# Performance work log

Measured on AMD Instinct MI355X. Metric: run time of the kernel, lower is better.

Reference implementation:

```python
import jax, jax.numpy as jnp
import numpy as np

N = 100000
E = 1600000
IN_C = 128
HID = 128
NUM_CLASSES = 16


def setup_inputs() -> dict:
    key = jax.random.key(0)
    ks = jax.random.split(key, 8)
    x = jax.random.normal(ks[0], (N, IN_C), dtype=jnp.float32)
    edge_index = jax.random.randint(ks[1], (2, E), 0, N, dtype=jnp.int64)
    s1 = 1.0 / np.sqrt(IN_C)
    s2 = 1.0 / np.sqrt(HID)
    W1 = jax.random.uniform(ks[2], (IN_C, HID), jnp.float32, -s1, s1)
    b1 = jnp.zeros((HID,), jnp.float32)
    W2 = jax.random.uniform(ks[3], (HID, HID), jnp.float32, -s2, s2)
    b2 = jnp.zeros((HID,), jnp.float32)
    Wl = jax.random.uniform(ks[4], (HID, NUM_CLASSES), jnp.float32, -s2, s2)
    bl = jax.random.uniform(ks[5], (NUM_CLASSES,), jnp.float32, -s2, s2)
    return {"x": x, "edge_index": edge_index, "W1": W1, "b1": b1,
            "W2": W2, "b2": b2, "Wl": Wl, "bl": bl}


def gcn_conv(x, src, dst, norm, W, b, n_nodes):
    # x: [N, F_in]; src/dst: [E+N] (self-loops appended); norm: [E+N]
    h = x @ W  # [N, F_out] -- transform first (F_out <= F_in style), then gather
    msg = h[src] * norm[:, None]  # [E+N, F_out] gathered, normalized messages
    out = jax.ops.segment_sum(msg, dst, num_segments=n_nodes)  # scatter-add
    return out + b


def reference(x, edge_index, W1, b1, W2, b2, Wl, bl):
    loop = jnp.arange(N, dtype=edge_index.dtype)
    src = jnp.concatenate([edge_index[0], loop])  # add self-loops
    dst = jnp.concatenate([edge_index[1], loop])
    # symmetric GCN normalization: deg computed on target side incl. self-loops
    deg = jax.ops.segment_sum(jnp.ones_like(dst, dtype=x.dtype), dst,
                              num_segments=N)
    dinv = jnp.where(deg > 0, jax.lax.rsqrt(deg), 0.0)
    norm = dinv[src] * dinv[dst]  # [E+N]

    h = jax.nn.relu(gcn_conv(x, src, dst, norm, W1, b1, N))
    h = jax.nn.relu(gcn_conv(h, src, dst, norm, W2, b2, N))
    logits = h @ Wl + bl
    return jax.nn.softmax(logits, axis=1)
```

## Files before the change

kernel.cpp:

```cpp
#include <hip/hip_runtime.h>
#include <hip/hip_fp16.h>

#define FDIM 128
#define NCLS 16

#define SCAN_T 256
#define SCAN_I 8
#define SCAN_CHUNK (SCAN_T * SCAN_I)

typedef _Float16 f16x8 __attribute__((ext_vector_type(8)));
typedef float f32x4 __attribute__((ext_vector_type(4)));

__global__ void k_count(const int* __restrict__ dst, int* cnt, int e) {
    int i = blockIdx.x * blockDim.x + threadIdx.x;
    if (i < e) atomicAdd(&cnt[dst[i]], 1);
}

__global__ __launch_bounds__(SCAN_T) void k_scan1(const int* __restrict__ cnt,
                                                  int* __restrict__ excl,
                                                  int* __restrict__ blockSum,
                                                  float* __restrict__ dinv, int n) {
    __shared__ int ts[SCAN_T];
    int b = blockIdx.x, t = threadIdx.x;
    int base = b * SCAN_CHUNK + t * SCAN_I;
    int v[SCAN_I];
    int s = 0;
    #pragma unroll
    for (int i = 0; i < SCAN_I; ++i) {
        int idx = base + i;
        v[i] = (idx < n) ? cnt[idx] : 0;
        if (idx < n) dinv[idx] = rsqrtf((float)(v[i] + 1));
        s += v[i];
    }
    ts[t] = s;
    __syncthreads();
    for (int off = 1; off < SCAN_T; off <<= 1) {
        int x = (t >= off) ? ts[t - off] : 0;
        __syncthreads();
        ts[t] += x;
        __syncthreads();
    }
    int ex = (t == 0) ? 0 : ts[t - 1];
    #pragma unroll
    for (int i = 0; i < SCAN_I; ++i) {
        int idx = base + i;
        if (idx < n) excl[idx] = ex;
        ex += v[i];
    }
    if (t == SCAN_T - 1) blockSum[b] = ts[SCAN_T - 1];
}

__global__ __launch_bounds__(1024) void k_scan2(int* blockSum, int* total, int nb) {
    __shared__ int ts[1024];
    int t = threadIdx.x;
    int v = (t < nb) ? blockSum[t] : 0;
    ts[t] = v;
    __syncthreads();
    for (int off = 1; off < 1024; off <<= 1) {
        int x = (t >= off) ? ts[t - off] : 0;
        __syncthreads();
        ts[t] += x;
        __syncthreads();
    }
    if (t < nb) blockSum[t] = (t == 0) ? 0 : ts[t - 1];
    if (t == 1023) *total = ts[1023];
}

__global__ void k_scan3(int* __restrict__ row_ptr, int* __restrict__ cursor,
                        const int* __restrict__ blockSum, const int* __restrict__ total,
                        int n) {
    int i = blockIdx.x * blockDim.x + threadIdx.x;
    if (i < n) {
        int v = row_ptr[i] + blockSum[i / SCAN_CHUNK];
        row_ptr[i] = v;
        cursor[i] = v;
    }
    if (i == 0) row_ptr[n] = *total;
}

__global__ void k_scatter(const int* __restrict__ src, const int* __restrict__ dst,
                          int* cursor, int* __restrict__ csr_off, int e) {
    int i = blockIdx.x * blockDim.x + threadIdx.x;
    if (i >= e) return;
    int pos = atomicAdd(&cursor[dst[i]], 1);
    csr_off[pos] = src[i] << 8;
}

__global__ __launch_bounds__(256) void k_prepw(const float* __restrict__ W1,
                                               const float* __restrict__ W2,
                                               __half* __restrict__ T1,
                                               __half* __restrict__ T2) {
    const float* W = (blockIdx.x == 0) ? W1 : W2;
    __half* T = (blockIdx.x == 0) ? T1 : T2;
    int t = threadIdx.x;
    for (int i = t; i < 128 * 32; i += 256) {
        int c = i >> 5, k4 = (i & 31) * 4;
        float a = W[(k4 + 0) * 128 + c];
        float b = W[(k4 + 1) * 128 + c];
        float d = W[(k4 + 2) * 128 + c];
        float f = W[(k4 + 3) * 128 + c];
        __half2 h0 = __float22half2_rn(make_float2(a, b));
        __half2 h1 = __float22half2_rn(make_float2(d, f));
        uint2 u;
        u.x = *reinterpret_cast<unsigned int*>(&h0);
        u.y = *reinterpret_cast<unsigned int*>(&h1);
        *reinterpret_cast<uint2*>(&T[c * 128 + k4]) = u;
    }
}

template <typename T>
__global__ __launch_bounds__(512) void k_gemm_mfma(const T* __restrict__ A,
                                                   const __half* __restrict__ WT,
                                                   const float* __restrict__ dinv,
                                                   __half* __restrict__ C, int n) {
    __shared__ _Float16 as[128 * 128];
    __shared__ _Float16 wt[128 * 128];
    int t = threadIdx.x;
    int r0 = blockIdx.x * 128;

    for (int i = t; i < 2048; i += 512) {
        int c = i >> 4, k8 = i & 15;
        uint4 u = reinterpret_cast<const uint4*>(WT)[i];
        int byte = (c * 256 + k8 * 16) ^ ((c & 7) << 4);
        *reinterpret_cast<uint4*>(reinterpret_cast<char*>(wt) + byte) = u;
    }

    if constexpr (sizeof(T) == 4) {
        for (int i = t; i < 128 * 16; i += 512) {
            int r = i >> 4, c8 = i & 15;
            float4 v0 = make_float4(0.f, 0.f, 0.f, 0.f);
            float4 v1 = make_float4(0.f, 0.f, 0.f, 0.f);
            if (r0 + r < n) {
                v0 = reinterpret_cast<const float4*>(A)[(size_t)(r0 + r) * 32 + c8 * 2];
                v1 = reinterpret_cast<const float4*>(A)[(size_t)(r0 + r) * 32 + c8 * 2 + 1];
            }
            __half2 h0 = __float22half2_rn(make_float2(v0.x, v0.y));
            __half2 h1 = __float22half2_rn(make_float2(v0.z, v0.w));
            __half2 h2 = __float22half2_rn(make_float2(v1.x, v1.y));
            __half2 h3 = __float22half2_rn(make_float2(v1.z, v1.w));
            uint4 u;
            u.x = *reinterpret_cast<unsigned int*>(&h0);
            u.y = *reinterpret_cast<unsigned int*>(&h1);
            u.z = *reinterpret_cast<unsigned int*>(&h2);
            u.w = *reinterpret_cast<unsigned int*>(&h3);
            int byte = (r * 256 + c8 * 16) ^ ((r & 7) << 4);
            *reinterpret_cast<uint4*>(reinterpret_cast<char*>(as) + byte) = u;
        }
    } else {
        for (int i = t; i < 128 * 16; i += 512) {
            int r = i >> 4, c8 = i & 15;
            uint4 u = make_uint4(0, 0, 0, 0);
            if (r0 + r < n)
                u = reinterpret_cast<const uint4*>(A)[(size_t)(r0 + r) * 16 + c8];
            int byte = (r * 256 + c8 * 16) ^ ((r & 7) << 4);
            *reinterpret_cast<uint4*>(reinterpret_cast<char*>(as) + byte) = u;
        }
    }
    __syncthreads();

    int w = t >> 6, l = t & 63;
    int lrow = l & 15, lk = l >> 4;
    int rw = w * 16;

    f16x8 afrag[4];
    #pragma unroll
    for (int ks = 0; ks < 4; ++ks) {
        int row = rw + lrow;
        int byte = (row * 256 + (ks * 4 + lk) * 16) ^ ((row & 7) << 4);
        afrag[ks] = *reinterpret_cast<const f16x8*>(reinterpret_cast<const char*>(as) + byte);
    }
    float dv[4];
    #pragma unroll
    for (int reg = 0; reg < 4; ++reg) {
        int rg = r0 + rw + lk * 4 + reg;
        dv[reg] = (rg < n) ? dinv[rg] : 0.f;
    }

    #pragma unroll
    for (int ct = 0; ct < 8; ++ct) {
        f32x4 acc = {0.f, 0.f, 0.f, 0.f};
        #pragma unroll
        for (int ks = 0; ks < 4; ++ks) {
            int c = ct * 16 + lrow;
            int byte = (c * 256 + (ks * 4 + lk) * 16) ^ ((c & 7) << 4);
            f16x8 bfrag = *reinterpret_cast<const f16x8*>(reinterpret_cast<const char*>(wt) + byte);
            acc = __builtin_amdgcn_mfma_f32_16x16x32_f16(afrag[ks], bfrag, acc, 0, 0, 0);
        }
        #pragma unroll
        for (int reg = 0; reg < 4; ++reg) {
            int rg = r0 + rw + lk * 4 + reg;
            if (rg < n)
                C[(size_t)rg * FDIM + ct * 16 + lrow] = __float2half(acc[reg] * dv[reg]);
        }
    }
}

template <bool FUSE>
__global__ __launch_bounds__(256) void k_agg2e(const __half* __restrict__ Y,
                                               const int* __restrict__ csr_off,
                                               const int* __restrict__ row_ptr,
                                               const float* __restrict__ dinv,
                                               const float* __restrict__ bias,
                                               const float* __restrict__ Wl,
                                               const float* __restrict__ bl,
                                               __half* __restrict__ hout,
                                               float* __restrict__ out, int n) {
    __shared__ float s_wl[NCLS * FDIM];
    __shared__ float s_bl[NCLS];
    if (FUSE) {
        for (int i = threadIdx.x; i < FDIM * NCLS / 4; i += 256) {
            int k = i >> 2, c4 = (i & 3) * 4;
            float4 v = reinterpret_cast<const float4*>(Wl)[i];
            s_wl[(c4 + 0) * FDIM + k] = v.x;
            s_wl[(c4 + 1) * FDIM + k] = v.y;
            s_wl[(c4 + 2) * FDIM + k] = v.z;
            s_wl[(c4 + 3) * FDIM + k] = v.w;
        }
        if (threadIdx.x < NCLS) s_bl[threadIdx.x] = bl[threadIdx.x];
        __syncthreads();
    }

    int node = blockIdx.x * 4 + (threadIdx.x >> 6);
    if (node >= n) return;
    int lane = threadIdx.x & 63;
    int half = lane >> 5, l32 = lane & 31;
    const char* Yb = reinterpret_cast<const char*>(Y);
    const char* lanebase = Yb + (l32 << 3);

    float a0 = 0.f, a1 = 0.f, a2 = 0.f, a3 = 0.f;
    int beg = row_ptr[node], end = row_ptr[node + 1];

    for (int j0 = beg; j0 < end; j0 += 64) {
        int cnt = min(64, end - j0);
        int myoff = (j0 + lane < end) ? csr_off[j0 + lane] : 0;
        int k = 0;
        for (; k + 8 <= cnt; k += 8) {
            uint2 u[4];
            #pragma unroll
            for (int i = 0; i < 4; ++i) {
                int oe = __builtin_amdgcn_readlane(myoff, k + 2 * i);
                int oo = __builtin_amdgcn_readlane(myoff, k + 2 * i + 1);
                int off = half ? oo : oe;
                u[i] = *reinterpret_cast<const uint2*>(lanebase + off);
            }
            __half2* p = reinterpret_cast<__half2*>(u);
            __half2 lo = __hadd2(__hadd2(p[0], p[2]), __hadd2(p[4], p[6]));
            __half2 hi = __hadd2(__hadd2(p[1], p[3]), __hadd2(p[5], p[7]));
            float2 flo = __half22float2(lo), fhi = __half22float2(hi);
            a0 += flo.x; a1 += flo.y; a2 += fhi.x; a3 += fhi.y;
        }
        for (; k + 2 <= cnt; k += 2) {
            int oe = __builtin_amdgcn_readlane(myoff, k);
            int oo = __builtin_amdgcn_readlane(myoff, k + 1);
            int off = half ? oo : oe;
            uint2 u = *reinterpret_cast<const uint2*>(lanebase + off);
            __half2* p = reinterpret_cast<__half2*>(&u);
            float2 flo = __half22float2(p[0]), fhi = __half22float2(p[1]);
            a0 += flo.x; a1 += flo.y; a2 += fhi.x; a3 += fhi.y;
        }
        if (k < cnt) {
            int o = __builtin_amdgcn_readlane(myoff, k);
            uint2 u = *reinterpret_cast<const uint2*>(lanebase + o);
            __half2* p = reinterpret_cast<__half2*>(&u);
            float sel = (half == 0) ? 1.0f : 0.0f;
            float2 flo = __half22float2(p[0]), fhi = __half22float2(p[1]);
            a0 += flo.x * sel; a1 += flo.y * sel;
            a2 += fhi.x * sel; a3 += fhi.y * sel;
        }
    }

    a0 += __shfl_xor(a0, 32, 64);
    a1 += __shfl_xor(a1, 32, 64);
    a2 += __shfl_xor(a2, 32, 64);
    a3 += __shfl_xor(a3, 32, 64);

    uint2 su = *reinterpret_cast<const uint2*>(Yb + ((size_t)node << 8) + (l32 << 3));
    __half2* sp = reinterpret_cast<__half2*>(&su);
    float2 slo = __half22float2(sp[0]), shi = __half22float2(sp[1]);
    a0 += slo.x; a1 += slo.y; a2 += shi.x; a3 += shi.y;

    float di = dinv[node];
    float4 b = *reinterpret_cast<const float4*>(bias + l32 * 4);
    float h0 = fmaxf(a0 * di + b.x, 0.f);
    float h1 = fmaxf(a1 * di + b.y, 0.f);
    float h2 = fmaxf(a2 * di + b.z, 0.f);
    float h3 = fmaxf(a3 * di + b.w, 0.f);

    if (!FUSE) {
        if (half == 0) {
            __half2 o0 = __float22half2_rn(make_float2(h0, h1));
            __half2 o1 = __float22half2_rn(make_float2(h2, h3));
            uint2 o;
            o.x = *reinterpret_cast<unsigned int*>(&o0);
            o.y = *reinterpret_cast<unsigned int*>(&o1);
            *reinterpret_cast<uint2*>(reinterpret_cast<char*>(hout) + ((size_t)node << 8) + (l32 << 3)) = o;
        }
    } else {
        float lg[NCLS];
        #pragma unroll
        for (int c = 0; c < NCLS; ++c) {
            float4 w4 = *reinterpret_cast<const float4*>(&s_wl[c * FDIM + l32 * 4]);
            lg[c] = h0 * w4.x + h1 * w4.y + h2 * w4.z + h3 * w4.w;
        }
        #pragma unroll
        for (int off = 1; off < 32; off <<= 1) {
            #pragma unroll
            for (int c = 0; c < NCLS; ++c) lg[c] += __shfl_xor(lg[c], off, 64);
        }
        #pragma unroll
        for (int c = 0; c < NCLS; ++c) lg[c] += s_bl[c];
        float m = lg[0];
        #pragma unroll
        for (int c = 1; c < NCLS; ++c) m = fmaxf(m, lg[c]);
        float ev[NCLS];
        float sum = 0.f;
        #pragma unroll
        for (int c = 0; c < NCLS; ++c) { ev[c] = __expf(lg[c] - m); sum += ev[c]; }
        float inv = 1.0f / sum;
        float mye = 0.f;
        #pragma unroll
        for (int c = 0; c < NCLS; ++c) if (lane == c) mye = ev[c];
        if (lane < NCLS) out[(size_t)node * NCLS + lane] = mye * inv;
    }
}

extern "C" void kernel_launch(void* const* d_in, const int* in_sizes, int n_in,
                              void* d_out, int out_size, void* d_ws, size_t ws_size,
                              hipStream_t stream) {
    const float* x  = (const float*)d_in[0];
    const int*   ei = (const int*)d_in[1];
    const float* W1 = (const float*)d_in[2];
    const float* b1 = (const float*)d_in[3];
    const float* W2 = (const float*)d_in[4];
    const float* b2 = (const float*)d_in[5];
    const float* Wl = (const float*)d_in[6];
    const float* bl = (const float*)d_in[7];
    float* out = (float*)d_out;

    int n = in_sizes[0] / FDIM;
    int e = in_sizes[1] / 2;
    const int* src = ei;
    const int* dst = ei + e;

    int nb = (n + SCAN_CHUNK - 1) / SCAN_CHUNK;

    float* dinv    = (float*)d_ws;
    int*   cnt     = (int*)(dinv + n);
    int*   row_ptr = cnt + n;
    int*   cursor  = row_ptr + n + 1;
    int*   blockSum= cursor + n;
    int*   total   = blockSum + 1024;
    int*   csr_off = total + 1;
    uintptr_t p = (uintptr_t)(csr_off + e);
    p = (p + 15) & ~(uintptr_t)15;
    __half* wt1 = (__half*)p;
    __half* wt2 = wt1 + 128 * 128;
    __half* bufA = wt2 + 128 * 128;
    __half* bufB = bufA + (size_t)n * FDIM;

    int bn = (n + 255) / 256;
    int be = (e + 255) / 256;

    hipMemsetAsync(cnt, 0, (size_t)n * sizeof(int), stream);
    k_prepw<<<2, 256, 0, stream>>>(W1, W2, wt1, wt2);
    k_count<<<be, 256, 0, stream>>>(dst, cnt, e);
    k_scan1<<<nb, SCAN_T, 0, stream>>>(cnt, row_ptr, blockSum, dinv, n);
    k_scan2<<<1, 1024, 0, stream>>>(blockSum, total, nb);
    k_scan3<<<bn, 256, 0, stream>>>(row_ptr, cursor, blockSum, total, n);
    k_scatter<<<be, 256, 0, stream>>>(src, dst, cursor, csr_off, e);

    int bg = (n + 127) / 128;
    int ba = (n + 3) / 4;

    k_gemm_mfma<float><<<bg, 512, 0, stream>>>(x, wt1, dinv, bufA, n);
    k_agg2e<false><<<ba, 256, 0, stream>>>(bufA, csr_off, row_ptr, dinv, b1, Wl, bl, bufB, out, n);

    k_gemm_mfma<__half><<<bg, 512, 0, stream>>>(bufB, wt2, dinv, bufA, n);
    k_agg2e<true><<<ba, 256, 0, stream>>>(bufA, csr_off, row_ptr, dinv, b2, Wl, bl, bufB, out, n);
}
```

Before: 478.0 us.

## Gather four edges per wavefront with 16-byte loads and fold weight prep into scan

The aggregation kernel now splits each 64-lane wavefront into four 16-lane groups, each loading a full 256-byte fp16 row with 16-byte loads. Four neighbors are processed at once instead of two, with a two-step xor-shuffle reduction across groups at the end. The goal is fewer, wider gather instructions and more memory-level parallelism per wave on the edge-gather path. Separately, the weight transpose/fp16 conversion kernel is merged into the single-block scan2 launch as extra blocks, removing one kernel launch. The tail handling duplicates loads for masked groups, and the logits reduction now uses 16-lane shuffles.

```diff
diff --git a/kernel.cpp b/kernel.cpp
--- a/kernel.cpp
+++ b/kernel.cpp
@@ -50,20 +50,42 @@
     if (t == SCAN_T - 1) blockSum[b] = ts[SCAN_T - 1];
 }
 
-__global__ __launch_bounds__(1024) void k_scan2(int* blockSum, int* total, int nb) {
-    __shared__ int ts[1024];
-    int t = threadIdx.x;
-    int v = (t < nb) ? blockSum[t] : 0;
-    ts[t] = v;
-    __syncthreads();
-    for (int off = 1; off < 1024; off <<= 1) {
-        int x = (t >= off) ? ts[t - off] : 0;
+__global__ __launch_bounds__(1024) void k_scan2_prepw(int* blockSum, int* total, int nb,
+                                                      const float* __restrict__ W1,
+                                                      const float* __restrict__ W2,
+                                                      __half* __restrict__ T1,
+                                                      __half* __restrict__ T2) {
+    if (blockIdx.x == 0) {
+        __shared__ int ts[1024];
+        int t = threadIdx.x;
+        int v = (t < nb) ? blockSum[t] : 0;
+        ts[t] = v;
         __syncthreads();
-        ts[t] += x;
-        __syncthreads();
-    }
-    if (t < nb) blockSum[t] = (t == 0) ? 0 : ts[t - 1];
-    if (t == 1023) *total = ts[1023];
+        for (int off = 1; off < 1024; off <<= 1) {
+            int x = (t >= off) ? ts[t - off] : 0;
+            __syncthreads();
+            ts[t] += x;
+            __syncthreads();
+        }
+        if (t < nb) blockSum[t] = (t == 0) ? 0 : ts[t - 1];
+        if (t == 1023) *total = ts[1023];
+    } else {
+        const float* W = (blockIdx.x == 1) ? W1 : W2;
+        __half* T = (blockIdx.x == 1) ? T1 : T2;
+        for (int i = threadIdx.x; i < 128 * 32; i += 1024) {
+            int c = i >> 5, k4 = (i & 31) * 4;
+            float a = W[(k4 + 0) * 128 + c];
+            float b = W[(k4 + 1) * 128 + c];
+            float d = W[(k4 + 2) * 128 + c];
+            float f = W[(k4 + 3) * 128 + c];
+            __half2 h0 = __float22half2_rn(make_float2(a, b));
+            __half2 h1 = __float22half2_rn(make_float2(d, f));
+            uint2 u;
+            u.x = *reinterpret_cast<unsigned int*>(&h0);
+            u.y = *reinterpret_cast<unsigned int*>(&h1);
+            *reinterpret_cast<uint2*>(&T[c * 128 + k4]) = u;
+        }
+    }
 }
 
 __global__ void k_scan3(int* __restrict__ row_ptr, int* __restrict__ cursor,
@@ -84,28 +106,6 @@
     if (i >= e) return;
     int pos = atomicAdd(&cursor[dst[i]], 1);
     csr_off[pos] = src[i] << 8;
-}
-
-__global__ __launch_bounds__(256) void k_prepw(const float* __restrict__ W1,
-                                               const float* __restrict__ W2,
-                                               __half* __restrict__ T1,
-                                               __half* __restrict__ T2) {
-    const float* W = (blockIdx.x == 0) ? W1 : W2;
-    __half* T = (blockIdx.x == 0) ? T1 : T2;
-    int t = threadIdx.x;
-    for (int i = t; i < 128 * 32; i += 256) {
-        int c = i >> 5, k4 = (i & 31) * 4;
-        float a = W[(k4 + 0) * 128 + c];
-        float b = W[(k4 + 1) * 128 + c];
-        float d = W[(k4 + 2) * 128 + c];
-        float f = W[(k4 + 3) * 128 + c];
-        __half2 h0 = __float22half2_rn(make_float2(a, b));
-        __half2 h1 = __float22half2_rn(make_float2(d, f));
-        uint2 u;
-        u.x = *reinterpret_cast<unsigned int*>(&h0);
-        u.y = *reinterpret_cast<unsigned int*>(&h1);
-        *reinterpret_cast<uint2*>(&T[c * 128 + k4]) = u;
-    }
 }
 
 template <typename T>
@@ -196,7 +196,7 @@
 }
 
 template <bool FUSE>
-__global__ __launch_bounds__(256) void k_agg2e(const __half* __restrict__ Y,
+__global__ __launch_bounds__(256) void k_agg4e(const __half* __restrict__ Y,
                                                const int* __restrict__ csr_off,
                                                const int* __restrict__ row_ptr,
                                                const float* __restrict__ dinv,
@@ -223,11 +223,11 @@
     int node = blockIdx.x * 4 + (threadIdx.x >> 6);
     if (node >= n) return;
     int lane = threadIdx.x & 63;
-    int half = lane >> 5, l32 = lane & 31;
+    int grp = lane >> 4, l16 = lane & 15;
     const char* Yb = reinterpret_cast<const char*>(Y);
-    const char* lanebase = Yb + (l32 << 3);
-
-    float a0 = 0.f, a1 = 0.f, a2 = 0.f, a3 = 0.f;
+    const char* lanebase = Yb + l16 * 16;
+
+    float2 A0 = {0.f, 0.f}, A1 = {0.f, 0.f}, A2 = {0.f, 0.f}, A3 = {0.f, 0.f};
     int beg = row_ptr[node], end = row_ptr[node + 1];
 
     for (int j0 = beg; j0 < end; j0 += 64) {
@@ -235,75 +235,98 @@
         int myoff = (j0 + lane < end) ? csr_off[j0 + lane] : 0;
         int k = 0;
         for (; k + 8 <= cnt; k += 8) {
-            uint2 u[4];
-            #pragma unroll
-            for (int i = 0; i < 4; ++i) {
-                int oe = __builtin_amdgcn_readlane(myoff, k + 2 * i);
-                int oo = __builtin_amdgcn_readlane(myoff, k + 2 * i + 1);
-                int off = half ? oo : oe;
-                u[i] = *reinterpret_cast<const uint2*>(lanebase + off);
-            }
-            __half2* p = reinterpret_cast<__half2*>(u);
-            __half2 lo = __hadd2(__hadd2(p[0], p[2]), __hadd2(p[4], p[6]));
-            __half2 hi = __hadd2(__hadd2(p[1], p[3]), __hadd2(p[5], p[7]));
-            float2 flo = __half22float2(lo), fhi = __half22float2(hi);
-            a0 += flo.x; a1 += flo.y; a2 += fhi.x; a3 += fhi.y;
-        }
-        for (; k + 2 <= cnt; k += 2) {
-            int oe = __builtin_amdgcn_readlane(myoff, k);
-            int oo = __builtin_amdgcn_readlane(myoff, k + 1);
-            int off = half ? oo : oe;
-            uint2 u = *reinterpret_cast<const uint2*>(lanebase + off);
+            int o1 = __shfl(myoff, k + grp, 64);
+            int o2 = __shfl(myoff, k + 4 + grp, 64);
+            uint4 u1 = *reinterpret_cast<const uint4*>(lanebase + o1);
+            uint4 u2 = *reinterpret_cast<const uint4*>(lanebase + o2);
+            __half2* p1 = reinterpret_cast<__half2*>(&u1);
+            __half2* p2 = reinterpret_cast<__half2*>(&u2);
+            __half2 s0 = __hadd2(p1[0], p2[0]);
+            __half2 s1 = __hadd2(p1[1], p2[1]);
+            __half2 s2 = __hadd2(p1[2], p2[2]);
+            __half2 s3 = __hadd2(p1[3], p2[3]);
+            float2 f0 = __half22float2(s0), f1 = __half22float2(s1);
+            float2 f2 = __half22float2(s2), f3 = __half22float2(s3);
+            A0.x += f0.x; A0.y += f0.y; A1.x += f1.x; A1.y += f1.y;
+            A2.x += f2.x; A2.y += f2.y; A3.x += f3.x; A3.y += f3.y;
+        }
+        for (; k + 4 <= cnt; k += 4) {
+            int o = __shfl(myoff, k + grp, 64);
+            uint4 u = *reinterpret_cast<const uint4*>(lanebase + o);
             __half2* p = reinterpret_cast<__half2*>(&u);
-            float2 flo = __half22float2(p[0]), fhi = __half22float2(p[1]);
-            a0 += flo.x; a1 += flo.y; a2 += fhi.x; a3 += fhi.y;
+            float2 f0 = __half22float2(p[0]), f1 = __half22float2(p[1]);
+            float2 f2 = __half22float2(p[2]), f3 = __half22float2(p[3]);
+            A0.x += f0.x; A0.y += f0.y; A1.x += f1.x; A1.y += f1.y;
+            A2.x += f2.x; A2.y += f2.y; A3.x += f3.x; A3.y += f3.y;
         }
         if (k < cnt) {
-            int o = __builtin_amdgcn_readlane(myoff, k);
-            uint2 u = *reinterpret_cast<const uint2*>(lanebase + o);
+            int rem = cnt - k;
+            int o = __shfl(myoff, k + min(grp, rem - 1), 64);
+            uint4 u = *reinterpret_cast<const uint4*>(lanebase + o);
             __half2* p = reinterpret_cast<__half2*>(&u);
-            float sel = (half == 0) ? 1.0f : 0.0f;
-            float2 flo = __half22float2(p[0]), fhi = __half22float2(p[1]);
-            a0 += flo.x * sel; a1 += flo.y * sel;
-            a2 += fhi.x * sel; a3 += fhi.y * sel;
-        }
-    }
-
-    a0 += __shfl_xor(a0, 32, 64);
-    a1 += __shfl_xor(a1, 32, 64);
-    a2 += __shfl_xor(a2, 32, 64);
-    a3 += __shfl_xor(a3, 32, 64);
-
-    uint2 su = *reinterpret_cast<const uint2*>(Yb + ((size_t)node << 8) + (l32 << 3));
-    __half2* sp = reinterpret_cast<__half2*>(&su);
-    float2 slo = __half22float2(sp[0]), shi = __half22float2(sp[1]);
-    a0 += slo.x; a1 += slo.y; a2 += shi.x; a3 += shi.y;
+            float sel = (grp < rem) ? 1.0f : 0.0f;
+            float2 f0 = __half22float2(p[0]), f1 = __half22float2(p[1]);
+            float2 f2 = __half22float2(p[2]), f3 = __half22float2(p[3]);
+            A0.x += f0.x * sel; A0.y += f0.y * sel;
+            A1.x += f1.x * sel; A1.y += f1.y * sel;
+            A2.x += f2.x * sel; A2.y += f2.y * sel;
+            A3.x += f3.x * sel; A3.y += f3.y * sel;
+        }
+    }
+
+    #pragma unroll
+    for (int off = 16; off <= 32; off <<= 1) {
+        A0.x += __shfl_xor(A0.x, off, 64); A0.y += __shfl_xor(A0.y, off, 64);
+        A1.x += __shfl_xor(A1.x, off, 64); A1.y += __shfl_xor(A1.y, off, 64);
+        A2.x += __shfl_xor(A2.x, off, 64); A2.y += __shfl_xor(A2.y, off, 64);
+        A3.x += __shfl_xor(A3.x, off, 64); A3.y += __shfl_xor(A3.y, off, 64);
+    }
+
+    {
+        uint4 u = *reinterpret_cast<const uint4*>(Yb + ((size_t)node << 8) + l16 * 16);
+        __half2* p = reinterpret_cast<__half2*>(&u);
+        float2 f0 = __half22float2(p[0]), f1 = __half22float2(p[1]);
+        float2 f2 = __half22float2(p[2]), f3 = __half22float2(p[3]);
+        A0.x += f0.x; A0.y += f0.y; A1.x += f1.x; A1.y += f1.y;
+        A2.x += f2.x; A2.y += f2.y; A3.x += f3.x; A3.y += f3.y;
+    }
 
     float di = dinv[node];
-    float4 b = *reinterpret_cast<const float4*>(bias + l32 * 4);
-    float h0 = fmaxf(a0 * di + b.x, 0.f);
-    float h1 = fmaxf(a1 * di + b.y, 0.f);
-    float h2 = fmaxf(a2 * di + b.z, 0.f);
-    float h3 = fmaxf(a3 * di + b.w, 0.f);
+    float4 ba = *reinterpret_cast<const float4*>(bias + l16 * 8);
+    float4 bb = *reinterpret_cast<const float4*>(bias + l16 * 8 + 4);
+    float h0 = fmaxf(A0.x * di + ba.x, 0.f);
+    float h1 = fmaxf(A0.y * di + ba.y, 0.f);
+    float h2 = fmaxf(A1.x * di + ba.z, 0.f);
+    float h3 = fmaxf(A1.y * di + ba.w, 0.f);
+    float h4 = fmaxf(A2.x * di + bb.x, 0.f);
+    float h5 = fmaxf(A2.y * di + bb.y, 0.f);
+    float h6 = fmaxf(A3.x * di + bb.z, 0.f);
+    float h7 = fmaxf(A3.y * di + bb.w, 0.f);
 
     if (!FUSE) {
-        if (half == 0) {
+        if (grp == 0) {
             __half2 o0 = __float22half2_rn(make_float2(h0, h1));
             __half2 o1 = __float22half2_rn(make_float2(h2, h3));
-            uint2 o;
+            __half2 o2 = __float22half2_rn(make_float2(h4, h5));
+            __half2 o3 = __float22half2_rn(make_float2(h6, h7));
+            uint4 o;
             o.x = *reinterpret_cast<unsigned int*>(&o0);
             o.y = *reinterpret_cast<unsigned int*>(&o1);
-            *reinterpret_cast<uint2*>(reinterpret_cast<char*>(hout) + ((size_t)node << 8) + (l32 << 3)) = o;
+            o.z = *reinterpret_cast<unsigned int*>(&o2);
+            o.w = *reinterpret_cast<unsigned int*>(&o3);
+            *reinterpret_cast<uint4*>(reinterpret_cast<char*>(hout) + ((size_t)node << 8) + l16 * 16) = o;
         }
     } else {
         float lg[NCLS];
         #pragma unroll
         for (int c = 0; c < NCLS; ++c) {
-            float4 w4 = *reinterpret_cast<const float4*>(&s_wl[c * FDIM + l32 * 4]);
-            lg[c] = h0 * w4.x + h1 * w4.y + h2 * w4.z + h3 * w4.w;
-        }
-        #pragma unroll
-        for (int off = 1; off < 32; off <<= 1) {
+            float4 wa = *reinterpret_cast<const float4*>(&s_wl[c * FDIM + l16 * 8]);
+            float4 wb = *reinterpret_cast<const float4*>(&s_wl[c * FDIM + l16 * 8 + 4]);
+            lg[c] = h0 * wa.x + h1 * wa.y + h2 * wa.z + h3 * wa.w +
+                    h4 * wb.x + h5 * wb.y + h6 * wb.z + h7 * wb.w;
+        }
+        #pragma unroll
+        for (int off = 1; off < 16; off <<= 1) {
             #pragma unroll
             for (int c = 0; c < NCLS; ++c) lg[c] += __shfl_xor(lg[c], off, 64);
         }
@@ -362,10 +385,9 @@
     int be = (e + 255) / 256;
 
     hipMemsetAsync(cnt, 0, (size_t)n * sizeof(int), stream);
-    k_prepw<<<2, 256, 0, stream>>>(W1, W2, wt1, wt2);
     k_count<<<be, 256, 0, stream>>>(dst, cnt, e);
     k_scan1<<<nb, SCAN_T, 0, stream>>>(cnt, row_ptr, blockSum, dinv, n);
-    k_scan2<<<1, 1024, 0, stream>>>(blockSum, total, nb);
+    k_scan2_prepw<<<3, 1024, 0, stream>>>(blockSum, total, nb, W1, W2, wt1, wt2);
     k_scan3<<<bn, 256, 0, stream>>>(row_ptr, cursor, blockSum, total, n);
     k_scatter<<<be, 256, 0, stream>>>(src, dst, cursor, csr_off, e);
 
@@ -373,8 +395,8 @@
     int ba = (n + 3) / 4;
 
     k_gemm_mfma<float><<<bg, 512, 0, stream>>>(x, wt1, dinv, bufA, n);
-    k_agg2e<false><<<ba, 256, 0, stream>>>(bufA, csr_off, row_ptr, dinv, b1, Wl, bl, bufB, out, n);
+    k_agg4e<false><<<ba, 256, 0, stream>>>(bufA, csr_off, row_ptr, dinv, b1, Wl, bl, bufB, out, n);
 
     k_gemm_mfma<__half><<<bg, 512, 0, stream>>>(bufB, wt2, dinv, bufA, n);
-    k_agg2e<true><<<ba, 256, 0, stream>>>(bufA, csr_off, row_ptr, dinv, b2, Wl, bl, bufB, out, n);
-}
+    k_agg4e<true><<<ba, 256, 0, stream>>>(bufA, csr_off, row_ptr, dinv, b2, Wl, bl, bufB, out, n);
+}
```

Result: slower. 489.0 us (+2.3%).
